# Kernel tuning notes

Measured on AMD Instinct MI355X. Metric: run time of the kernel, lower is better.

The kernel has to match this reference:

```python
import jax, jax.numpy as jnp
import numpy as np

B, T, D = 8, 2048, 1024

def _xavier(key, shape):
    fan_in, fan_out = shape[1], shape[0]
    limit = float(np.sqrt(6.0 / (fan_in + fan_out)))
    return jax.random.uniform(key, shape, jnp.float32, -limit, limit)

def setup_inputs() -> dict:
    key = jax.random.key(0)
    ks = jax.random.split(key, 6)
    x = jax.random.normal(ks[0], (B, T, D), jnp.float32)
    return {
        "x": x,
        "h0": jnp.zeros((B, D), jnp.float32),
        "W_in": _xavier(ks[1], (D, D)),      # in_proj.weight [d_inner, dim]
        "W_alpha": _xavier(ks[2], (D, D)),
        "d_alpha": jnp.full((D,), 0.1, jnp.float32),
        "b_alpha": jnp.full((D,), 2.0, jnp.float32),
        "W_x": _xavier(ks[3], (D, D)),
        "b_v": jnp.zeros((D,), jnp.float32),
        "W_out": _xavier(ks[4], (D, D)),     # out_proj.weight [dim, d_inner]
    }

def _silu(u):
    return u * jax.nn.sigmoid(u)

def reference(x, h0, W_in, W_alpha, d_alpha, b_alpha, W_x, b_v, W_out):
    # in_proj + SiLU: [B,T,D]
    x_proj = _silu(jnp.einsum('btd,ed->bte', x, W_in))
    # to [T,B,D] for the scan
    x_rnn = jnp.transpose(x_proj, (1, 0, 2))
    # precompute per-step gate/value GEMM contributions (as in torch ref)
    alpha_x = jnp.einsum('tbd,ed->tbe', x_rnn, W_alpha)          # [T,B,D]
    v_all = jnp.tanh(jnp.einsum('tbd,ed->tbe', x_rnn, W_x) + b_v)  # [T,B,D]

    def step(h_prev, inputs):
        ax_t, v_t = inputs
        alpha = jax.nn.sigmoid(ax_t + d_alpha * h_prev + b_alpha)
        h_new = alpha * h_prev + (1.0 - alpha) * v_t
        out_t = h_new * _silu(h_new)
        return h_new, out_t

    h_final, cell_out = jax.lax.scan(step, h0, (alpha_x, v_all))  # cell_out: [T,B,D]
    cell_out = jnp.transpose(cell_out, (1, 0, 2))                 # [B,T,D]
    output = jnp.einsum('btd,ed->bte', cell_out, W_out)
    return output, h_final
```

## Files before the change

kernel.cpp:

```cpp
#include <hip/hip_runtime.h>
#include <hip/hip_bf16.h>

typedef __attribute__((ext_vector_type(8))) short short8;
typedef __attribute__((ext_vector_type(4))) short short4v;
typedef __attribute__((ext_vector_type(4))) float f32x4;

#define Dk 1024
#define TT 2048
#define BB 8
#define MROWS (BB * TT)
#define LOG2E 1.44269504088896f

#if defined(__has_builtin)
#if __has_builtin(__builtin_amdgcn_rcpf)
#define FAST_RCP(x) __builtin_amdgcn_rcpf(x)
#endif
#if __has_builtin(__builtin_amdgcn_exp2f)
#define FAST_EXP2(x) __builtin_amdgcn_exp2f(x)
#endif
#endif
#ifndef FAST_RCP
#define FAST_RCP(x) (1.f / (x))
#endif
#ifndef FAST_EXP2
#define FAST_EXP2(x) exp2f(x)
#endif

__device__ __forceinline__ void gload_lds16(const void* g, void* l) {
    __builtin_amdgcn_global_load_lds(
        (const __attribute__((address_space(1))) void*)g,
        (__attribute__((address_space(3))) void*)l, 16, 0, 0);
}

__device__ __forceinline__ float sigmoidf_fast(float x) {
    return FAST_RCP(1.f + FAST_EXP2(-x * LOG2E));
}

__device__ __forceinline__ unsigned short bf16_bits(float x) {
    union { __hip_bfloat16 h; unsigned short u; } c;
    c.h = __float2bfloat16(x);
    return c.u;
}

__global__ __launch_bounds__(256)
void cvt_all(const float* __restrict__ x,
             const float* __restrict__ w0, const float* __restrict__ w1,
             const float* __restrict__ w2, const float* __restrict__ w3,
             __hip_bfloat16* __restrict__ xo,
             __hip_bfloat16* __restrict__ o0, __hip_bfloat16* __restrict__ o1,
             __hip_bfloat16* __restrict__ o2, __hip_bfloat16* __restrict__ o3)
{
    const int bid = blockIdx.x;
    const float* in;
    __hip_bfloat16* out;
    int base;
    if (bid < 16384) {
        in = x; out = xo; base = bid * 1024;
    } else {
        const int wbid  = bid - 16384;
        const int which = wbid >> 10;
        in  = which == 0 ? w0 : which == 1 ? w1 : which == 2 ? w2 : w3;
        out = which == 0 ? o0 : which == 1 ? o1 : which == 2 ? o2 : o3;
        base = (wbid & 1023) * 1024;
    }
    const int i = base + threadIdx.x * 4;
    const float4 v = *(const float4*)(in + i);
    __hip_bfloat16 tmp[4];
    tmp[0] = __float2bfloat16(v.x);
    tmp[1] = __float2bfloat16(v.y);
    tmp[2] = __float2bfloat16(v.z);
    tmp[3] = __float2bfloat16(v.w);
    *(short4v*)(out + i) = *(const short4v*)tmp;
}

template<int EPI>
__global__ __launch_bounds__(256)
void gemm_bt(const __hip_bfloat16* __restrict__ A,
             const __hip_bfloat16* __restrict__ Bw,
             const float* __restrict__ bias,
             void* __restrict__ CoutV)
{
    __shared__ __hip_bfloat16 sA[2][128 * 32];
    __shared__ __hip_bfloat16 sB[2][128 * 32];

    const int tid  = threadIdx.x;
    const int bid  = blockIdx.x;
    const int nbid = (bid & 7) * 128 + (bid >> 3);
    const int tn   = nbid & 7;
    const int tm   = nbid >> 3;
    const int lane = tid & 63;
    const int w    = tid >> 6;
    const int wr   = (w >> 1) * 64;
    const int wc   = (w & 1) * 64;
    const int l15  = lane & 15;
    const int lq   = lane >> 4;

    f32x4 acc[4][4];
#pragma unroll
    for (int m = 0; m < 4; ++m)
#pragma unroll
        for (int n = 0; n < 4; ++n)
            acc[m][n] = (f32x4){0.f, 0.f, 0.f, 0.f};

    const size_t baseA = (size_t)(tm * 128) * Dk;
    const size_t baseB = (size_t)(tn * 128) * Dk;

    auto stage = [&](int k0, int buf) {
#pragma unroll
        for (int i = 0; i < 2; ++i) {
            const int li  = i * 256 + tid;
            const int row = li >> 2;
            const int cb  = li & 3;
            const size_t go = (size_t)row * Dk + k0 + cb * 8;
            gload_lds16(A  + baseA + go, (char*)sA[buf] + li * 16);
            gload_lds16(Bw + baseB + go, (char*)sB[buf] + li * 16);
        }
    };

    stage(0, 0);
    __syncthreads();

    int buf = 0;
    for (int k0 = 0; k0 < Dk; k0 += 32) {
        if (k0 + 32 < Dk) stage(k0 + 32, buf ^ 1);

        short8 af[4], bfr[4];
#pragma unroll
        for (int m = 0; m < 4; ++m)
            af[m] = *(const short8*)(sA[buf] + (wr + m * 16 + l15) * 32 + lq * 8);
#pragma unroll
        for (int n = 0; n < 4; ++n)
            bfr[n] = *(const short8*)(sB[buf] + (wc + n * 16 + l15) * 32 + lq * 8);

#pragma unroll
        for (int m = 0; m < 4; ++m)
#pragma unroll
            for (int n = 0; n < 4; ++n)
                acc[m][n] = __builtin_amdgcn_mfma_f32_16x16x32_bf16(
                    af[m], bfr[n], acc[m][n], 0, 0, 0);

        __syncthreads();
        buf ^= 1;
    }

#pragma unroll
    for (int m = 0; m < 4; ++m) {
#pragma unroll
        for (int n = 0; n < 4; ++n) {
            const int col = tn * 128 + wc + n * 16 + l15;
            float bv_ = 0.f;
            if (EPI == 6 || EPI == 7) bv_ = bias[col];
#pragma unroll
            for (int j = 0; j < 4; ++j) {
                const int rowl = wr + m * 16 + lq * 4 + j;
                const size_t idx = (size_t)(tm * 128 + rowl) * Dk + col;
                const float xv = acc[m][n][j];
                if constexpr (EPI == 0) {
                    ((__hip_bfloat16*)CoutV)[idx] =
                        __float2bfloat16(xv * sigmoidf_fast(xv));
                } else if constexpr (EPI == 1) {
                    ((float*)CoutV)[idx] = xv;
                } else if constexpr (EPI == 6) {
                    const float e = FAST_EXP2(-(xv + bv_) * LOG2E);
                    ((unsigned short*)CoutV)[idx * 2] = bf16_bits(e);
                } else {
                    const float y = xv + bv_;
                    const float e = FAST_EXP2(fabsf(y) * (2.f * LOG2E));
                    float t = 1.f - 2.f * FAST_RCP(e + 1.f);
                    t = copysignf(t, y);
                    ((unsigned short*)CoutV)[idx * 2 + 1] = bf16_bits(t);
                }
            }
        }
    }
}

__global__ __launch_bounds__(64)
void scan_kernel(const unsigned int* __restrict__ EV,
                 const float* __restrict__ h0,
                 const float* __restrict__ dal,
                 __hip_bfloat16* __restrict__ hout, float* __restrict__ hfin)
{
    constexpr int CH  = 32;
    constexpr int NCH = TT / CH;
    __shared__ __align__(16) unsigned int lEV[2][CH * 64];

    const int tid = threadIdx.x;
    const int bx  = blockIdx.x;
    const int b   = bx >> 4;
    const int d0  = (bx & 15) * 64;
    const int d   = d0 + tid;
    const int g   = b * Dk + d;

    float nl2 = -dal[d] * LOG2E;
    if (fabsf(nl2) < 1e-18f) nl2 = -1e-18f;
    const float inv_nl2 = 1.f / nl2;
    float ht = h0[g] * nl2;

    const size_t sbase = (size_t)b * TT * Dk + d0;

    const int sl = tid >> 4;
    const int co = (tid & 15) * 4;

    auto issue = [&](int ck, int buf) {
#pragma unroll
        for (int grp = 0; grp < 8; ++grp) {
            const size_t off = sbase + (size_t)(ck * CH + grp * 4 + sl) * Dk + co;
            gload_lds16(EV + off, (void*)&lEV[buf][grp * 256]);
        }
    };

    issue(0, 0);
    asm volatile("s_waitcnt vmcnt(0)" ::: "memory");
    __builtin_amdgcn_sched_barrier(0);

    for (int k = 0; k < NCH; ++k) {
        const int buf = k & 1;
        if (k + 1 < NCH) issue(k + 1, buf ^ 1);
        __builtin_amdgcn_sched_barrier(0);

        const size_t cbase = sbase + (size_t)(k * CH) * Dk + tid;
#pragma unroll
        for (int s = 0; s < CH; ++s) {
            const unsigned int wv = lEV[buf][s * 64 + tid];
            const float E  = __uint_as_float(wv << 16);
            const float Vt = __uint_as_float(wv & 0xffff0000u) * nl2;
            const float u  = FAST_EXP2(ht);
            const float al = FAST_RCP(fmaf(E, u, 1.f));
            ht = fmaf(al, ht - Vt, Vt);
            hout[cbase + (size_t)s * Dk] = __float2bfloat16(ht * inv_nl2);
        }
        __builtin_amdgcn_sched_barrier(0);
        if (k + 1 < NCH) {
            asm volatile("s_waitcnt vmcnt(32)" ::: "memory");
        }
        __builtin_amdgcn_sched_barrier(0);
    }

    hfin[g] = ht * inv_nl2;
}

__global__ __launch_bounds__(256)
void gpass(const __hip_bfloat16* __restrict__ hin,
           __hip_bfloat16* __restrict__ cell, int n)
{
    const int stride = gridDim.x * 256 * 8;
    for (int i = (blockIdx.x * 256 + threadIdx.x) * 8; i < n; i += stride) {
        const short8 v = *(const short8*)(hin + i);
        short8 r;
#pragma unroll
        for (int j = 0; j < 8; ++j) {
            const float x = __uint_as_float(((unsigned int)(unsigned short)v[j]) << 16);
            const float s = sigmoidf_fast(x);
            r[j] = (short)bf16_bits(x * x * s);
        }
        *(short8*)(cell + i) = r;
    }
}

extern "C" void kernel_launch(void* const* d_in, const int* in_sizes, int n_in,
                              void* d_out, int out_size, void* d_ws, size_t ws_size,
                              hipStream_t stream)
{
    const float* x     = (const float*)d_in[0];
    const float* h0    = (const float*)d_in[1];
    const float* W_in  = (const float*)d_in[2];
    const float* W_al  = (const float*)d_in[3];
    const float* d_al  = (const float*)d_in[4];
    const float* b_al  = (const float*)d_in[5];
    const float* W_x   = (const float*)d_in[6];
    const float* b_v   = (const float*)d_in[7];
    const float* W_out = (const float*)d_in[8];

    float* out  = (float*)d_out;
    float* hfin = out + (size_t)MROWS * Dk;

    char* ws = (char*)d_ws;
    const size_t bfBuf = (size_t)MROWS * Dk * sizeof(__hip_bfloat16);
    const size_t wBuf  = (size_t)Dk * Dk * sizeof(__hip_bfloat16);

    __hip_bfloat16* xb    = (__hip_bfloat16*)(ws);
    __hip_bfloat16* Winb  = (__hip_bfloat16*)(ws + bfBuf);
    __hip_bfloat16* Walb  = (__hip_bfloat16*)(ws + bfBuf + wBuf);
    __hip_bfloat16* Wxb   = (__hip_bfloat16*)(ws + bfBuf + 2 * wBuf);
    __hip_bfloat16* Woutb = (__hip_bfloat16*)(ws + bfBuf + 3 * wBuf);
    char* rest = ws + bfBuf + 4 * wBuf;
    __hip_bfloat16* xproj = (__hip_bfloat16*)rest;
    unsigned int*   EVb   = (unsigned int*)(rest + bfBuf);

    __hip_bfloat16* hbuf  = xb;
    __hip_bfloat16* cellb = xproj;

    dim3 blk(256);
    cvt_all<<<dim3(16384 + 4096), blk, 0, stream>>>(
        x, W_in, W_al, W_x, W_out, xb, Winb, Walb, Wxb, Woutb);

    dim3 grid(1024);
    gemm_bt<0><<<grid, blk, 0, stream>>>(xb,    Winb,  nullptr, xproj);
    gemm_bt<6><<<grid, blk, 0, stream>>>(xproj, Walb,  b_al,    EVb);
    gemm_bt<7><<<grid, blk, 0, stream>>>(xproj, Wxb,   b_v,     EVb);
    scan_kernel<<<dim3(128), dim3(64), 0, stream>>>(EVb, h0, d_al, hbuf, hfin);
    gpass<<<dim3(2048), blk, 0, stream>>>(hbuf, cellb, MROWS * Dk);
    gemm_bt<1><<<grid, blk, 0, stream>>>(cellb, Woutb, nullptr, out);
}
```

Before: 300.4 us.

## Replace GEMM with 256x256 tiles, triple-buffered swizzled LDS and phased staging

Replaces the 128x128-tile, 256-thread GEMM with a 256x256-tile, 512-thread kernel. It uses three LDS buffers with XOR-swizzled layout to avoid bank conflicts, prefetches two k-steps ahead in two phases with explicit vmcnt waits, and sets MFMA priority with s_setprio. The larger tiles raise data reuse per global load and cut the grid to 256 blocks. In exchange each thread holds twice as many accumulators, which adds register pressure and a risk of lower occupancy or tail imbalance across CUs.

```diff
diff --git a/kernel.cpp b/kernel.cpp
--- a/kernel.cpp
+++ b/kernel.cpp
@@ -74,86 +74,131 @@
 }
 
 template<int EPI>
-__global__ __launch_bounds__(256)
-void gemm_bt(const __hip_bfloat16* __restrict__ A,
+__global__ __launch_bounds__(512, 2)
+void gemm256(const __hip_bfloat16* __restrict__ A,
              const __hip_bfloat16* __restrict__ Bw,
              const float* __restrict__ bias,
              void* __restrict__ CoutV)
 {
-    __shared__ __hip_bfloat16 sA[2][128 * 32];
-    __shared__ __hip_bfloat16 sB[2][128 * 32];
+    __shared__ __align__(16) char lds[3 * 32768];
 
     const int tid  = threadIdx.x;
     const int bid  = blockIdx.x;
-    const int nbid = (bid & 7) * 128 + (bid >> 3);
-    const int tn   = nbid & 7;
-    const int tm   = nbid >> 3;
+    const int nbid = (bid & 7) * 32 + (bid >> 3);
+    const int tn   = nbid & 3;
+    const int tm   = nbid >> 2;
     const int lane = tid & 63;
     const int w    = tid >> 6;
-    const int wr   = (w >> 1) * 64;
-    const int wc   = (w & 1) * 64;
+    const int wm   = w >> 2;
+    const int wn   = w & 3;
     const int l15  = lane & 15;
     const int lq   = lane >> 4;
 
-    f32x4 acc[4][4];
-#pragma unroll
-    for (int m = 0; m < 4; ++m)
+    const size_t baseA = (size_t)(tm * 256) * Dk;
+    const size_t baseB = (size_t)(tn * 256) * Dk;
+
+    int offA[8], offB[4];
+#pragma unroll
+    for (int m = 0; m < 8; ++m) {
+        const int row = wm * 128 + m * 16 + l15;
+        offA[m] = (row * 4 + (lq ^ (row & 3))) * 16;
+    }
+#pragma unroll
+    for (int n = 0; n < 4; ++n) {
+        const int row = wn * 64 + n * 16 + l15;
+        offB[n] = 16384 + (row * 4 + (lq ^ (row & 3))) * 16;
+    }
+
+    auto stagePh = [&](int kt, char* dst, int phase) {
+#pragma unroll
+        for (int j = 0; j < 2; ++j) {
+            const int slot = (phase * 2 + j) * 512 + tid;
+            const int s    = slot & 1023;
+            const int row  = s >> 2;
+            const int cb   = (s & 3) ^ (row & 3);
+            const __hip_bfloat16* src =
+                ((slot >> 10) ? Bw + baseB : A + baseA)
+                + (size_t)row * Dk + kt * 32 + cb * 8;
+            gload_lds16(src, dst + slot * 16);
+        }
+    };
+
+    f32x4 acc[8][4];
+#pragma unroll
+    for (int m = 0; m < 8; ++m)
 #pragma unroll
         for (int n = 0; n < 4; ++n)
             acc[m][n] = (f32x4){0.f, 0.f, 0.f, 0.f};
 
-    const size_t baseA = (size_t)(tm * 128) * Dk;
-    const size_t baseB = (size_t)(tn * 128) * Dk;
-
-    auto stage = [&](int k0, int buf) {
-#pragma unroll
-        for (int i = 0; i < 2; ++i) {
-            const int li  = i * 256 + tid;
-            const int row = li >> 2;
-            const int cb  = li & 3;
-            const size_t go = (size_t)row * Dk + k0 + cb * 8;
-            gload_lds16(A  + baseA + go, (char*)sA[buf] + li * 16);
-            gload_lds16(Bw + baseB + go, (char*)sB[buf] + li * 16);
-        }
-    };
-
-    stage(0, 0);
-    __syncthreads();
-
-    int buf = 0;
-    for (int k0 = 0; k0 < Dk; k0 += 32) {
-        if (k0 + 32 < Dk) stage(k0 + 32, buf ^ 1);
-
-        short8 af[4], bfr[4];
+    char* b0 = lds;
+    char* b1 = lds + 32768;
+    char* b2 = lds + 65536;
+
+    stagePh(0, b0, 0); stagePh(0, b0, 1);
+    stagePh(1, b1, 0); stagePh(1, b1, 1);
+    asm volatile("s_waitcnt vmcnt(4)" ::: "memory");
+    __builtin_amdgcn_s_barrier();
+
+    char* cbuf = b0;
+    char* nbuf = b1;
+    char* sbuf = b2;
+
+    for (int t = 0; t < 32; ++t) {
+        short8 af[4], af2[4], bfr[4];
+
+#pragma unroll
+        for (int n = 0; n < 4; ++n)
+            bfr[n] = *(const short8*)(cbuf + offB[n]);
 #pragma unroll
         for (int m = 0; m < 4; ++m)
-            af[m] = *(const short8*)(sA[buf] + (wr + m * 16 + l15) * 32 + lq * 8);
-#pragma unroll
-        for (int n = 0; n < 4; ++n)
-            bfr[n] = *(const short8*)(sB[buf] + (wc + n * 16 + l15) * 32 + lq * 8);
-
+            af[m] = *(const short8*)(cbuf + offA[m]);
+        if (t < 30) stagePh(t + 2, sbuf, 0);
+        __builtin_amdgcn_s_barrier();
+        __builtin_amdgcn_s_setprio(1);
 #pragma unroll
         for (int m = 0; m < 4; ++m)
 #pragma unroll
             for (int n = 0; n < 4; ++n)
                 acc[m][n] = __builtin_amdgcn_mfma_f32_16x16x32_bf16(
                     af[m], bfr[n], acc[m][n], 0, 0, 0);
-
-        __syncthreads();
-        buf ^= 1;
-    }
-
-#pragma unroll
-    for (int m = 0; m < 4; ++m) {
+        __builtin_amdgcn_s_setprio(0);
+        __builtin_amdgcn_s_barrier();
+
+#pragma unroll
+        for (int m = 0; m < 4; ++m)
+            af2[m] = *(const short8*)(cbuf + offA[4 + m]);
+        if (t < 30) stagePh(t + 2, sbuf, 1);
+        __builtin_amdgcn_s_barrier();
+        __builtin_amdgcn_s_setprio(1);
+#pragma unroll
+        for (int m = 0; m < 4; ++m)
+#pragma unroll
+            for (int n = 0; n < 4; ++n)
+                acc[4 + m][n] = __builtin_amdgcn_mfma_f32_16x16x32_bf16(
+                    af2[m], bfr[n], acc[4 + m][n], 0, 0, 0);
+        __builtin_amdgcn_s_setprio(0);
+
+        if (t < 30) {
+            asm volatile("s_waitcnt vmcnt(4)" ::: "memory");
+        } else if (t == 30) {
+            asm volatile("s_waitcnt vmcnt(0)" ::: "memory");
+        }
+        if (t < 31) __builtin_amdgcn_s_barrier();
+
+        char* tmp = cbuf; cbuf = nbuf; nbuf = sbuf; sbuf = tmp;
+    }
+
+#pragma unroll
+    for (int m = 0; m < 8; ++m) {
 #pragma unroll
         for (int n = 0; n < 4; ++n) {
-            const int col = tn * 128 + wc + n * 16 + l15;
+            const int col = tn * 256 + wn * 64 + n * 16 + l15;
             float bv_ = 0.f;
             if (EPI == 6 || EPI == 7) bv_ = bias[col];
 #pragma unroll
             for (int j = 0; j < 4; ++j) {
-                const int rowl = wr + m * 16 + lq * 4 + j;
-                const size_t idx = (size_t)(tm * 128 + rowl) * Dk + col;
+                const int rowg = tm * 256 + wm * 128 + m * 16 + lq * 4 + j;
+                const size_t idx = (size_t)rowg * Dk + col;
                 const float xv = acc[m][n][j];
                 if constexpr (EPI == 0) {
                     ((__hip_bfloat16*)CoutV)[idx] =
@@ -166,9 +211,9 @@
                 } else {
                     const float y = xv + bv_;
                     const float e = FAST_EXP2(fabsf(y) * (2.f * LOG2E));
-                    float t = 1.f - 2.f * FAST_RCP(e + 1.f);
-                    t = copysignf(t, y);
-                    ((unsigned short*)CoutV)[idx * 2 + 1] = bf16_bits(t);
+                    float tv = 1.f - 2.f * FAST_RCP(e + 1.f);
+                    tv = copysignf(tv, y);
+                    ((unsigned short*)CoutV)[idx * 2 + 1] = bf16_bits(tv);
                 }
             }
         }
@@ -295,11 +340,11 @@
     cvt_all<<<dim3(16384 + 4096), blk, 0, stream>>>(
         x, W_in, W_al, W_x, W_out, xb, Winb, Walb, Wxb, Woutb);
 
-    dim3 grid(1024);
-    gemm_bt<0><<<grid, blk, 0, stream>>>(xb,    Winb,  nullptr, xproj);
-    gemm_bt<6><<<grid, blk, 0, stream>>>(xproj, Walb,  b_al,    EVb);
-    gemm_bt<7><<<grid, blk, 0, stream>>>(xproj, Wxb,   b_v,     EVb);
+    dim3 ggrid(256), gblk(512);
+    gemm256<0><<<ggrid, gblk, 0, stream>>>(xb,    Winb,  nullptr, xproj);
+    gemm256<6><<<ggrid, gblk, 0, stream>>>(xproj, Walb,  b_al,    EVb);
+    gemm256<7><<<ggrid, gblk, 0, stream>>>(xproj, Wxb,   b_v,     EVb);
     scan_kernel<<<dim3(128), dim3(64), 0, stream>>>(EVb, h0, d_al, hbuf, hfin);
     gpass<<<dim3(2048), blk, 0, stream>>>(hbuf, cellb, MROWS * Dk);
-    gemm_bt<1><<<grid, blk, 0, stream>>>(cellb, Woutb, nullptr, out);
-}
+    gemm256<1><<<ggrid, gblk, 0, stream>>>(cellb, Woutb, nullptr, out);
+}
```

Result: faster. 279.7 us (-6.9%).
